# Performance work log

Measured on AMD Instinct MI355X. Metric: run time of the kernel, lower is better.

## Reference

```python
import jax, jax.numpy as jnp
import numpy as np

HEADS = 6
DIM_HEAD = 64
SCALE = DIM_HEAD ** -0.5
BN_EPS = 1e-5


def _dw_pw(x, w_dw, gamma, beta, mean, var, w_pw, stride):
    """Depthwise 3x3 conv (groups=C) -> BatchNorm (inference) -> 1x1 pointwise conv."""
    C = x.shape[1]
    y = jax.lax.conv_general_dilated(
        x, w_dw, window_strides=(stride, stride), padding=((1, 1), (1, 1)),
        dimension_numbers=('NCHW', 'OIHW', 'NCHW'), feature_group_count=C)
    inv = gamma / jnp.sqrt(var + BN_EPS)
    y = y * inv[None, :, None, None] + (beta - mean * inv)[None, :, None, None]
    # 1x1 conv as einsum: w_pw is [O, C]
    return jnp.einsum('bchw,oc->bohw', y, w_pw)


def setup_inputs() -> dict:
    key = jax.random.key(0)
    ks = jax.random.split(key, 10)
    B, C, H, W = 32, 384, 32, 32
    inner = HEADS * DIM_HEAD  # 384
    ws = 0.05  # weight scale to keep attention logits sane
    return {
        'x': jax.random.normal(ks[0], (B, C, H, W), jnp.float32),
        'q_dw': jax.random.normal(ks[1], (C, 1, 3, 3), jnp.float32) * ws,
        'q_gamma': jnp.ones((C,), jnp.float32),
        'q_beta': jnp.zeros((C,), jnp.float32),
        'q_mean': jax.random.normal(ks[2], (C,), jnp.float32) * 0.1,
        'q_var': jax.random.uniform(ks[3], (C,), jnp.float32) + 0.5,
        'q_pw': jax.random.normal(ks[4], (inner, C), jnp.float32) * ws,
        'kv_dw': jax.random.normal(ks[5], (C, 1, 3, 3), jnp.float32) * ws,
        'kv_gamma': jnp.ones((C,), jnp.float32),
        'kv_beta': jnp.zeros((C,), jnp.float32),
        'kv_mean': jax.random.normal(ks[6], (C,), jnp.float32) * 0.1,
        'kv_var': jax.random.uniform(ks[7], (C,), jnp.float32) + 0.5,
        'kv_pw': jax.random.normal(ks[8], (2 * inner, C), jnp.float32) * ws,
        'out_w': jax.random.normal(ks[9], (C, inner), jnp.float32) * ws,
        'out_b': jnp.zeros((C,), jnp.float32),
    }


def reference(x, q_dw, q_gamma, q_beta, q_mean, q_var, q_pw,
              kv_dw, kv_gamma, kv_beta, kv_mean, kv_var, kv_pw,
              out_w, out_b):
    B, C, H, W = x.shape
    h, d = HEADS, DIM_HEAD
    # Q at full resolution, K/V spatially downsampled (stride 2)
    q = _dw_pw(x, q_dw, q_gamma, q_beta, q_mean, q_var, q_pw, stride=1)   # [B, h*d, H, W]
    kv = _dw_pw(x, kv_dw, kv_gamma, kv_beta, kv_mean, kv_var, kv_pw, stride=2)  # [B, 2*h*d, Hk, Wk]
    k, v = jnp.split(kv, 2, axis=1)
    Hk, Wk = k.shape[2], k.shape[3]
    # 'b (h d) x y -> b h (x y) d'
    q = q.reshape(B, h, d, H * W).transpose(0, 1, 3, 2)
    k = k.reshape(B, h, d, Hk * Wk).transpose(0, 1, 3, 2)
    v = v.reshape(B, h, d, Hk * Wk).transpose(0, 1, 3, 2)
    dots = jnp.einsum('bhid,bhjd->bhij', q, k) * SCALE  # [B, h, HW, HkWk]
    attn = jax.nn.softmax(dots, axis=-1)
    out = jnp.einsum('bhij,bhjd->bhid', attn, v)        # [B, h, HW, d]
    # 'b h (x y) d -> b (h d) x y'
    out = out.transpose(0, 1, 3, 2).reshape(B, h * d, H, W)
    # final 1x1 conv projection (dropout is identity, p=0)
    return jnp.einsum('bchw,oc->bohw', out, out_w) + out_b[None, :, None, None]
```

## Files before the change

### kernel.cpp

```cpp
#include <hip/hip_runtime.h>
#include <hip/hip_bf16.h>

#define CIN 384
#define PQ 1024
#define PKV 256
#define HEADS 6
#define DH 64
#define INNER 384
#define ATTN_SCALE 0.125f

typedef __hip_bfloat16 bf16;
typedef unsigned short ushort;
typedef __bf16 bf16x8 __attribute__((ext_vector_type(8)));
typedef float floatx4 __attribute__((ext_vector_type(4)));
typedef short shortx4 __attribute__((ext_vector_type(4)));

#if __has_builtin(__builtin_amdgcn_mfma_f32_16x16x16bf16_1k)
#define HAVE_MFMA16 1
#endif

__device__ __forceinline__ float b2f(bf16 v) { return __bfloat162float(v); }
__device__ __forceinline__ bf16 f2b(float v) { return __float2bfloat16(v); }
__device__ __forceinline__ ushort f2bu(float v) { bf16 h = __float2bfloat16(v); return *(ushort*)&h; }
__device__ __forceinline__ float ldf(const void* p, size_t i, int isbf) {
    return isbf ? __bfloat162float(((const bf16*)p)[i]) : ((const float*)p)[i];
}
__device__ __forceinline__ void dma16(const bf16* g, bf16* l) {
    __builtin_amdgcn_global_load_lds(
        (const __attribute__((address_space(1))) unsigned int*)g,
        (__attribute__((address_space(3))) unsigned int*)l, 16, 0, 0);
}

__global__ void detect_kernel(const unsigned int* __restrict__ x, int* __restrict__ flag) {
    if (threadIdx.x == 0 && blockIdx.x == 0) {
        int cnt = 0;
        for (int i = 0; i < 64; i++) {
            unsigned int e = (x[i] >> 7) & 0xFFu;
            if (e >= 100u && e <= 140u) cnt++;
        }
        *flag = (cnt >= 48) ? 1 : 0;
    }
}

__global__ void wconv_kernel(const void* __restrict__ w0, const void* __restrict__ w1,
                             const void* __restrict__ w2, bf16* __restrict__ dst,
                             const int* __restrict__ flagp) {
    int isbf = *flagp;
    const int n0 = INNER * CIN, n1 = 2 * INNER * CIN, n2 = INNER * CIN;
    int i = blockIdx.x * 256 + threadIdx.x;
    int total = n0 + n1 + n2;
    for (; i < total; i += gridDim.x * 256) {
        float v;
        if (i < n0) v = ldf(w0, i, isbf);
        else if (i < n0 + n1) v = ldf(w1, i - n0, isbf);
        else v = ldf(w2, i - n0 - n1, isbf);
        dst[i] = f2b(v);
    }
}

template <int STRIDE, int HO, int WO>
__global__ __launch_bounds__(256) void dw_bn_kernel(
        const void* __restrict__ x, const void* __restrict__ wdw,
        const void* __restrict__ gamma, const void* __restrict__ beta,
        const void* __restrict__ mean, const void* __restrict__ var,
        bf16* __restrict__ yt, const int* __restrict__ flagp) {
    constexpr int IN_ROWS = (8 - 1) * STRIDE + 3;
    constexpr int RL = 37;
    constexpr int PT = 8 * WO;
    constexpr unsigned XSZ = 32u * IN_ROWS * RL * 4;
    constexpr unsigned OSZ = (unsigned)PT * 40 * 2;
    __shared__ __align__(16) char smem[XSZ > OSZ ? XSZ : OSZ];
    float (*xin)[IN_ROWS][RL] = (float (*)[IN_ROWS][RL])smem;
    ushort (*outt)[40] = (ushort (*)[40])smem;

    int isbf = *flagp;
    int rg = blockIdx.x;
    int c0 = blockIdx.y * 32;
    int b  = blockIdx.z;
    int tid = threadIdx.x;
    int ri0 = rg * 8 * STRIDE - 1;

    for (int e = tid; e < 32 * IN_ROWS; e += 256) {
        int i = e % IN_ROWS, cc = e / IN_ROWS;
        xin[cc][i][0] = 0.f;
        xin[cc][i][33] = 0.f;
    }

    const int NCHUNK = 32 * IN_ROWS * 4;
    for (int ch = tid; ch < NCHUNK; ch += 256) {
        int wc = ch & 3;
        int t  = ch >> 2;
        int i  = t % IN_ROWS;
        int cc = t / IN_ROWS;
        int row = ri0 + i;
        float f[8];
        if (row >= 0 && row < 32) {
            size_t goff = ((size_t)(b * CIN + c0 + cc) * 32 + row) * 32 + wc * 8;
            if (isbf) {
                uint4 v = *(const uint4*)((const bf16*)x + goff);
                const ushort* u = (const ushort*)&v;
#pragma unroll
                for (int j = 0; j < 8; j++) f[j] = __uint_as_float((unsigned)u[j] << 16);
            } else {
                float4 v0 = *(const float4*)((const float*)x + goff);
                float4 v1 = *(const float4*)((const float*)x + goff + 4);
                f[0] = v0.x; f[1] = v0.y; f[2] = v0.z; f[3] = v0.w;
                f[4] = v1.x; f[5] = v1.y; f[6] = v1.z; f[7] = v1.w;
            }
        } else {
#pragma unroll
            for (int j = 0; j < 8; j++) f[j] = 0.f;
        }
        float* dst = &xin[cc][i][1 + wc * 8];
#pragma unroll
        for (int j = 0; j < 8; j++) dst[j] = f[j];
    }

    int cc = tid & 31;
    int g  = tid >> 5;
    int c  = c0 + cc;
    float w9[9];
#pragma unroll
    for (int k = 0; k < 9; k++) w9[k] = ldf(wdw, c * 9 + k, isbf);
    float inv  = ldf(gamma, c, isbf) * rsqrtf(ldf(var, c, isbf) + 1e-5f);
    float bias = ldf(beta, c, isbf) - ldf(mean, c, isbf) * inv;
    __syncthreads();

    const float* xr0 = xin[cc][g * STRIDE + 0];
    const float* xr1 = xin[cc][g * STRIDE + 1];
    const float* xr2 = xin[cc][g * STRIDE + 2];
    float o[WO];
    if (STRIDE == 1) {
        float a0 = xr0[0], a1 = xr0[1];
        float b0 = xr1[0], b1 = xr1[1];
        float q0 = xr2[0], q1 = xr2[1];
#pragma unroll
        for (int wo = 0; wo < WO; wo++) {
            float a2 = xr0[wo + 2], b2 = xr1[wo + 2], q2 = xr2[wo + 2];
            float acc = w9[0] * a0 + w9[1] * a1 + w9[2] * a2
                      + w9[3] * b0 + w9[4] * b1 + w9[5] * b2
                      + w9[6] * q0 + w9[7] * q1 + w9[8] * q2;
            o[wo] = acc * inv + bias;
            a0 = a1; a1 = a2; b0 = b1; b1 = b2; q0 = q1; q1 = q2;
        }
    } else {
        float a0 = xr0[0], b0 = xr1[0], q0 = xr2[0];
#pragma unroll
        for (int wo = 0; wo < WO; wo++) {
            float a1 = xr0[2 * wo + 1], a2 = xr0[2 * wo + 2];
            float b1 = xr1[2 * wo + 1], b2 = xr1[2 * wo + 2];
            float q1 = xr2[2 * wo + 1], q2 = xr2[2 * wo + 2];
            float acc = w9[0] * a0 + w9[1] * a1 + w9[2] * a2
                      + w9[3] * b0 + w9[4] * b1 + w9[5] * b2
                      + w9[6] * q0 + w9[7] * q1 + w9[8] * q2;
            o[wo] = acc * inv + bias;
            a0 = a2; b0 = b2; q0 = q2;
        }
    }
    __syncthreads();

#pragma unroll
    for (int wo = 0; wo < WO; wo++) outt[g * WO + wo][cc] = f2bu(o[wo]);
    __syncthreads();

    const size_t pbase = (size_t)b * (HO * WO) + (size_t)rg * 8 * WO;
    for (int chk = tid; chk < PT * 4; chk += 256) {
        int k = chk & 3, p = chk >> 2;
        uint4 v = *(const uint4*)&outt[p][k * 8];
        *(uint4*)(yt + (pbase + p) * CIN + c0 + k * 8) = v;
    }
}

template <int P, int MODE>
__global__ __launch_bounds__(256, 2) void mfma_pw(
        const bf16* __restrict__ wt, const bf16* __restrict__ yt,
        const void* __restrict__ bias, void* __restrict__ out0,
        bf16* __restrict__ out1, int O, const int* __restrict__ flagp) {
    __shared__ __align__(16) bf16 As[2][4096];
    __shared__ __align__(16) bf16 Bs[2][4096];
    int tid = threadIdx.x;
    int wave = tid >> 6, lane = tid & 63;
    int l15 = lane & 15, quad = lane >> 4;
    int wm = wave & 1, wn = wave >> 1;
    int b = blockIdx.z;
    int p0 = blockIdx.x * 128;
    int o0 = blockIdx.y * 128;

    const bf16* asrc = yt + ((size_t)b * P + p0) * CIN;
    const bf16* bsrc = wt + (size_t)o0 * CIN;

    int srow = (lane >> 2);
    int sc   = lane & 3;
    auto stage = [&](int step, int buf) {
#pragma unroll
        for (int it = 0; it < 2; it++) {
            int row = wave * 32 + it * 16 + srow;
            int g = sc ^ (row & 3);
            size_t goff = (size_t)row * CIN + step * 32 + g * 8;
            dma16(asrc + goff, &As[buf][(wave * 2 + it) * 512]);
            dma16(bsrc + goff, &Bs[buf][(wave * 2 + it) * 512]);
        }
    };

    floatx4 acc[4][4];
#pragma unroll
    for (int pt = 0; pt < 4; pt++)
#pragma unroll
        for (int ot = 0; ot < 4; ot++) acc[pt][ot] = (floatx4){0.f, 0.f, 0.f, 0.f};

    stage(0, 0);
    __syncthreads();
    for (int s = 0; s < CIN / 32; s++) {
        int buf = s & 1;
        if (s < CIN / 32 - 1) stage(s + 1, buf ^ 1);
        bf16x8 af[4], bw[4];
        int slot = (quad ^ (l15 & 3)) * 8;
#pragma unroll
        for (int pt = 0; pt < 4; pt++)
            af[pt] = *(const bf16x8*)&As[buf][(wm * 64 + pt * 16 + l15) * 32 + slot];
#pragma unroll
        for (int ot = 0; ot < 4; ot++)
            bw[ot] = *(const bf16x8*)&Bs[buf][(wn * 64 + ot * 16 + l15) * 32 + slot];
#pragma unroll
        for (int pt = 0; pt < 4; pt++)
#pragma unroll
            for (int ot = 0; ot < 4; ot++)
                acc[pt][ot] = __builtin_amdgcn_mfma_f32_16x16x32_bf16(af[pt], bw[ot], acc[pt][ot], 0, 0, 0);
        __syncthreads();
    }

    int pw0 = p0 + wm * 64, ow0 = o0 + wn * 64;
    if (MODE == 2) {
        int isbf = *flagp;
#pragma unroll
        for (int ot = 0; ot < 4; ot++) {
            int o = ow0 + ot * 16 + l15;
            float bv = ldf(bias, o, isbf);
#pragma unroll
            for (int pt = 0; pt < 4; pt++) {
                int p = pw0 + pt * 16 + quad * 4;
                size_t idx = ((size_t)b * O + o) * P + p;
                if (!isbf) {
                    float4 v4 = {acc[pt][ot][0] + bv, acc[pt][ot][1] + bv,
                                 acc[pt][ot][2] + bv, acc[pt][ot][3] + bv};
                    *(float4*)((float*)out0 + idx) = v4;
                } else {
                    ushort4 u4 = {f2bu(acc[pt][ot][0] + bv), f2bu(acc[pt][ot][1] + bv),
                                  f2bu(acc[pt][ot][2] + bv), f2bu(acc[pt][ot][3] + bv)};
                    *(ushort4*)((bf16*)out0 + idx) = u4;
                }
            }
        }
    } else if (MODE == 0) {
#pragma unroll
        for (int ot = 0; ot < 4; ot++) {
            int o = ow0 + ot * 16 + l15;
            int h = o >> 6, d = o & 63;
            bf16* base = (bf16*)out0 + ((size_t)(b * HEADS + h) * P) * 64 + d;
#pragma unroll
            for (int pt = 0; pt < 4; pt++)
#pragma unroll
                for (int r = 0; r < 4; r++)
                    base[(size_t)(pw0 + pt * 16 + quad * 4 + r) * 64] = f2b(acc[pt][ot][r]);
        }
    } else {
#pragma unroll
        for (int ot = 0; ot < 4; ot++) {
            int o = ow0 + ot * 16 + l15;
            if (o < INNER) {
                int h = o >> 6, d = o & 63;
                bf16* base = (bf16*)out0 + ((size_t)(b * HEADS + h) * P) * 64 + d;
#pragma unroll
                for (int pt = 0; pt < 4; pt++)
#pragma unroll
                    for (int r = 0; r < 4; r++)
                        base[(size_t)(pw0 + pt * 16 + quad * 4 + r) * 64] = f2b(acc[pt][ot][r]);
            } else {
                int ch = o - INNER;
                bf16* base = out1 + ((size_t)b * INNER + ch) * PKV;
#pragma unroll
                for (int pt = 0; pt < 4; pt++)
#pragma unroll
                    for (int r = 0; r < 4; r++)
                        base[pw0 + pt * 16 + quad * 4 + r] = f2b(acc[pt][ot][r]);
            }
        }
    }
}

__global__ __launch_bounds__(256, 2) void attn_kernel(
        const bf16* __restrict__ qalt, const bf16* __restrict__ kalt,
        const bf16* __restrict__ valt, bf16* __restrict__ ao) {
    __shared__ __align__(16) bf16 Kl[16384];
    __shared__ __align__(16) bf16 Vl[16384];
    __shared__ __align__(16) ushort Ot[4][16][80];
    int tid = threadIdx.x;
    int wave = tid >> 6, lane = tid & 63;
    int l15 = lane & 15, quad = lane >> 4;
    int blk = blockIdx.x;
    int swz = (blk & 7) * 96 + (blk >> 3);
    int seg = swz & 3;
    int bh  = swz >> 2;
    int b = bh / HEADS, h = bh % HEADS;

    const bf16* qbase = qalt + (size_t)(b * HEADS + h) * PQ * DH;
    const bf16* kbase = kalt + (size_t)(b * HEADS + h) * PKV * DH;
    const bf16* vbase = valt + ((size_t)b * INNER + h * DH) * PKV;

    {
        int j = lane >> 3, cs = lane & 7;
#pragma unroll
        for (int it = 0; it < 8; it++) {
            int jr = (wave * 8 + it) * 8 + j;
            int g = cs ^ (jr & 7);
            dma16(kbase + (size_t)jr * 64 + g * 8, &Kl[(wave * 8 + it) * 512]);
        }
        int d = lane >> 5, cs2 = lane & 31;
#pragma unroll
        for (int it = 0; it < 8; it++) {
            int dr = (wave * 8 + it) * 2 + d;
            int g = cs2 ^ (dr & 15);
            dma16(vbase + (size_t)dr * 256 + g * 8, &Vl[(wave * 8 + it) * 512]);
        }
    }

    int p0 = seg * 256 + wave * 16;
    const bf16* qrow = qbase + (size_t)(p0 + l15) * DH + quad * 8;
    bf16x8 qc0 = *(const bf16x8*)qrow;
    bf16x8 qc1 = *(const bf16x8*)(qrow + 32);
    __syncthreads();

#pragma unroll
    for (int t = 0; t < 4; t++) {
        bf16x8 qn0 = qc0, qn1 = qc1;
        if (t < 3) {
            const bf16* qr = qrow + (size_t)(t + 1) * 64 * DH;
            qn0 = *(const bf16x8*)qr;
            qn1 = *(const bf16x8*)(qr + 32);
        }

        floatx4 s[16];
#pragma unroll
        for (int jt = 0; jt < 16; jt++) s[jt] = (floatx4){0.f, 0.f, 0.f, 0.f};
#pragma unroll
        for (int jt = 0; jt < 16; jt++) {
            int j = jt * 16 + l15;
            bf16x8 k0 = *(const bf16x8*)&Kl[j * 64 + (quad ^ (j & 7)) * 8];
            bf16x8 k1 = *(const bf16x8*)&Kl[j * 64 + ((4 + quad) ^ (j & 7)) * 8];
            s[jt] = __builtin_amdgcn_mfma_f32_16x16x32_bf16(k0, qc0, s[jt], 0, 0, 0);
            s[jt] = __builtin_amdgcn_mfma_f32_16x16x32_bf16(k1, qc1, s[jt], 0, 0, 0);
        }

        float mx = s[0][0];
#pragma unroll
        for (int jt = 0; jt < 16; jt++)
#pragma unroll
            for (int r = 0; r < 4; r++) mx = fmaxf(mx, s[jt][r]);
        mx = fmaxf(mx, __shfl_xor(mx, 16, 64));
        mx = fmaxf(mx, __shfl_xor(mx, 32, 64));
        float sm = 0.f;
#pragma unroll
        for (int jt = 0; jt < 16; jt++)
#pragma unroll
            for (int r = 0; r < 4; r++) {
                float e = __expf((s[jt][r] - mx) * ATTN_SCALE);
                s[jt][r] = e;
                sm += e;
            }
        sm += __shfl_xor(sm, 16, 64);
        sm += __shfl_xor(sm, 32, 64);
        float pinv = 1.f / sm;

        floatx4 oacc[4];
#pragma unroll
        for (int nt = 0; nt < 4; nt++) oacc[nt] = (floatx4){0.f, 0.f, 0.f, 0.f};
#ifdef HAVE_MFMA16
#pragma unroll
        for (int jt = 0; jt < 16; jt++) {
            shortx4 pa;
#pragma unroll
            for (int r = 0; r < 4; r++) pa[r] = (short)f2bu(s[jt][r] * pinv);
#pragma unroll
            for (int nt = 0; nt < 4; nt++) {
                int d = nt * 16 + l15;
                shortx4 bv = *(const shortx4*)&Vl[d * 256 +
                        ((jt * 2 + (quad >> 1)) ^ (d & 15)) * 8 + (quad & 1) * 4];
                oacc[nt] = __builtin_amdgcn_mfma_f32_16x16x16bf16_1k(pa, bv, oacc[nt], 0, 0, 0);
            }
        }
#else
#pragma unroll
        for (int kk = 0; kk < 8; kk++) {
            unsigned Ad0 = ((unsigned)f2bu(s[2 * kk][1] * pinv) << 16) | f2bu(s[2 * kk][0] * pinv);
            unsigned Ad1 = ((unsigned)f2bu(s[2 * kk][3] * pinv) << 16) | f2bu(s[2 * kk][2] * pinv);
            unsigned Bd0 = ((unsigned)f2bu(s[2 * kk + 1][1] * pinv) << 16) | f2bu(s[2 * kk + 1][0] * pinv);
            unsigned Bd1 = ((unsigned)f2bu(s[2 * kk + 1][3] * pinv) << 16) | f2bu(s[2 * kk + 1][2] * pinv);
            int srcA = l15 + ((quad & 1) << 5);
            unsigned dw[4];
#pragma unroll
            for (int i = 0; i < 4; i++) {
                int srcl = srcA + ((i >> 1) << 4);
                unsigned ta = (i & 1) ? __shfl((int)Ad1, srcl, 64) : __shfl((int)Ad0, srcl, 64);
                unsigned tb = (i & 1) ? __shfl((int)Bd1, srcl, 64) : __shfl((int)Bd0, srcl, 64);
                dw[i] = (quad >> 1) ? tb : ta;
            }
            union { unsigned u[4]; bf16x8 v; } pc;
            pc.u[0] = dw[0]; pc.u[1] = dw[1]; pc.u[2] = dw[2]; pc.u[3] = dw[3];
#pragma unroll
            for (int nt = 0; nt < 4; nt++) {
                int d = nt * 16 + l15;
                bf16x8 bv = *(const bf16x8*)&Vl[d * 256 + ((kk * 4 + quad) ^ (d & 15)) * 8];
                oacc[nt] = __builtin_amdgcn_mfma_f32_16x16x32_bf16(pc.v, bv, oacc[nt], 0, 0, 0);
            }
        }
#endif

#pragma unroll
        for (int nt = 0; nt < 4; nt++)
#pragma unroll
            for (int r = 0; r < 4; r++)
                Ot[wave][quad * 4 + r][nt * 16 + l15] = f2bu(oacc[nt][r]);
        int row = lane >> 2, d0 = (lane & 3) * 16;
        uint4 ld0 = *(const uint4*)&Ot[wave][row][d0];
        uint4 ld1 = *(const uint4*)&Ot[wave][row][d0 + 8];
        bf16* dst = ao + ((size_t)b * PQ + p0 + t * 64 + row) * INNER + h * DH + d0;
        *(uint4*)dst = ld0;
        *(uint4*)(dst + 8) = ld1;

        qc0 = qn0; qc1 = qn1;
    }
}

extern "C" void kernel_launch(void* const* d_in, const int* in_sizes, int n_in,
                              void* d_out, int out_size, void* d_ws, size_t ws_size,
                              hipStream_t stream) {
    const void* x        = d_in[0];
    const void* q_dw     = d_in[1];
    const void* q_gamma  = d_in[2];
    const void* q_beta   = d_in[3];
    const void* q_mean   = d_in[4];
    const void* q_var    = d_in[5];
    const void* q_pw     = d_in[6];
    const void* kv_dw    = d_in[7];
    const void* kv_gamma = d_in[8];
    const void* kv_beta  = d_in[9];
    const void* kv_mean  = d_in[10];
    const void* kv_var   = d_in[11];
    const void* kv_pw    = d_in[12];
    const void* out_w    = d_in[13];
    const void* out_b    = d_in[14];

    int* flag = (int*)d_ws;
    bf16* pool = (bf16*)((char*)d_ws + 256);
    bf16* yqt  = pool;
    bf16* ykvt = yqt  + (size_t)32 * 1024 * 384;
    bf16* qalt = ykvt + (size_t)32 * 256 * 384;
    bf16* kalt = qalt + (size_t)32 * 6 * 1024 * 64;
    bf16* valt = kalt + (size_t)32 * 6 * 256 * 64;
    bf16* wbf  = valt + (size_t)32 * 384 * 256;
    bf16* qpw_bf = wbf;
    bf16* kvpw_bf = wbf + (size_t)INNER * CIN;
    bf16* outw_bf = kvpw_bf + (size_t)2 * INNER * CIN;
    bf16* aob  = yqt;

    detect_kernel<<<1, 64, 0, stream>>>((const unsigned int*)x, flag);
    wconv_kernel<<<576, 256, 0, stream>>>(q_pw, kv_pw, out_w, wbf, flag);
    dw_bn_kernel<1, 32, 32><<<dim3(4, 12, 32), 256, 0, stream>>>(x, q_dw, q_gamma, q_beta, q_mean, q_var, yqt, flag);
    dw_bn_kernel<2, 16, 16><<<dim3(2, 12, 32), 256, 0, stream>>>(x, kv_dw, kv_gamma, kv_beta, kv_mean, kv_var, ykvt, flag);
    mfma_pw<1024, 0><<<dim3(8, 3, 32), 256, 0, stream>>>(qpw_bf, yqt, nullptr, qalt, nullptr, INNER, flag);
    mfma_pw<256, 1><<<dim3(2, 6, 32), 256, 0, stream>>>(kvpw_bf, ykvt, nullptr, kalt, valt, 2 * INNER, flag);
    attn_kernel<<<768, 256, 0, stream>>>(qalt, kalt, valt, aob);
    mfma_pw<1024, 2><<<dim3(8, 3, 32), 256, 0, stream>>>(outw_bf, aob, out_b, d_out, nullptr, CIN, flag);
}
```

Baseline: 241.5 us.

## Inline dtype probe, deepen GEMM K-step, and restructure attention with global K loads

Removes the separate detect kernel and has each kernel run the dtype probe inline, which saves one launch. The pointwise GEMM now stages 64-wide K slices with an 8-way swizzle, halving the number of barrier iterations. The attention kernel drops the K shared-memory copy and reads K straight from global memory. It doubles the grid to 1536 blocks with fewer query tiles each and raises occupancy to 3 blocks per CU. It also switches the softmax to exp2 with a folded scale and packs P using v_cvt_pk_bf16 plus permlane32_swap. The inline probe adds redundant reads of 64 words in every block, and reading K from global memory relies on cache hits.

```diff
diff --git a/kernel.cpp b/kernel.cpp
--- a/kernel.cpp
+++ b/kernel.cpp
@@ -13,11 +13,6 @@
 typedef unsigned short ushort;
 typedef __bf16 bf16x8 __attribute__((ext_vector_type(8)));
 typedef float floatx4 __attribute__((ext_vector_type(4)));
-typedef short shortx4 __attribute__((ext_vector_type(4)));
-
-#if __has_builtin(__builtin_amdgcn_mfma_f32_16x16x16bf16_1k)
-#define HAVE_MFMA16 1
-#endif
 
 __device__ __forceinline__ float b2f(bf16 v) { return __bfloat162float(v); }
 __device__ __forceinline__ bf16 f2b(float v) { return __float2bfloat16(v); }
@@ -30,22 +25,37 @@
         (const __attribute__((address_space(1))) unsigned int*)g,
         (__attribute__((address_space(3))) unsigned int*)l, 16, 0, 0);
 }
-
-__global__ void detect_kernel(const unsigned int* __restrict__ x, int* __restrict__ flag) {
-    if (threadIdx.x == 0 && blockIdx.x == 0) {
-        int cnt = 0;
-        for (int i = 0; i < 64; i++) {
-            unsigned int e = (x[i] >> 7) & 0xFFu;
-            if (e >= 100u && e <= 140u) cnt++;
-        }
-        *flag = (cnt >= 48) ? 1 : 0;
-    }
+__device__ __forceinline__ int probe_isbf(const void* x) {
+    const unsigned* u = (const unsigned*)x;
+    int cnt = 0;
+    for (int i = 0; i < 64; i++) {
+        unsigned e = (u[i] >> 7) & 0xFFu;
+        cnt += (e >= 100u && e <= 140u) ? 1 : 0;
+    }
+    return cnt >= 48 ? 1 : 0;
+}
+__device__ __forceinline__ unsigned cvtpk(float lo, float hi) {
+    unsigned r;
+    asm("v_cvt_pk_bf16_f32 %0, %1, %2" : "=v"(r) : "v"(lo), "v"(hi));
+    return r;
+}
+__device__ __forceinline__ void halfswap(unsigned a, unsigned b, unsigned& lo, unsigned& hi) {
+#if __has_builtin(__builtin_amdgcn_permlane32_swap)
+    auto r = __builtin_amdgcn_permlane32_swap(a, b, false, false);
+    lo = r[0]; hi = r[1];
+#else
+    unsigned ax = (unsigned)__shfl_xor((int)a, 32, 64);
+    unsigned bx = (unsigned)__shfl_xor((int)b, 32, 64);
+    bool lower = (threadIdx.x & 32) == 0;
+    lo = lower ? a : bx;
+    hi = lower ? ax : b;
+#endif
 }
 
 __global__ void wconv_kernel(const void* __restrict__ w0, const void* __restrict__ w1,
                              const void* __restrict__ w2, bf16* __restrict__ dst,
-                             const int* __restrict__ flagp) {
-    int isbf = *flagp;
+                             const void* __restrict__ xprobe) {
+    int isbf = probe_isbf(xprobe);
     const int n0 = INNER * CIN, n1 = 2 * INNER * CIN, n2 = INNER * CIN;
     int i = blockIdx.x * 256 + threadIdx.x;
     int total = n0 + n1 + n2;
@@ -63,7 +73,7 @@
         const void* __restrict__ x, const void* __restrict__ wdw,
         const void* __restrict__ gamma, const void* __restrict__ beta,
         const void* __restrict__ mean, const void* __restrict__ var,
-        bf16* __restrict__ yt, const int* __restrict__ flagp) {
+        bf16* __restrict__ yt) {
     constexpr int IN_ROWS = (8 - 1) * STRIDE + 3;
     constexpr int RL = 37;
     constexpr int PT = 8 * WO;
@@ -73,7 +83,7 @@
     float (*xin)[IN_ROWS][RL] = (float (*)[IN_ROWS][RL])smem;
     ushort (*outt)[40] = (ushort (*)[40])smem;
 
-    int isbf = *flagp;
+    int isbf = probe_isbf(x);
     int rg = blockIdx.x;
     int c0 = blockIdx.y * 32;
     int b  = blockIdx.z;
@@ -175,9 +185,9 @@
 __global__ __launch_bounds__(256, 2) void mfma_pw(
         const bf16* __restrict__ wt, const bf16* __restrict__ yt,
         const void* __restrict__ bias, void* __restrict__ out0,
-        bf16* __restrict__ out1, int O, const int* __restrict__ flagp) {
-    __shared__ __align__(16) bf16 As[2][4096];
-    __shared__ __align__(16) bf16 Bs[2][4096];
+        bf16* __restrict__ out1, int O, const void* __restrict__ xprobe) {
+    __shared__ __align__(16) bf16 As[2][8192];
+    __shared__ __align__(16) bf16 Bs[2][8192];
     int tid = threadIdx.x;
     int wave = tid >> 6, lane = tid & 63;
     int l15 = lane & 15, quad = lane >> 4;
@@ -189,16 +199,16 @@
     const bf16* asrc = yt + ((size_t)b * P + p0) * CIN;
     const bf16* bsrc = wt + (size_t)o0 * CIN;
 
-    int srow = (lane >> 2);
-    int sc   = lane & 3;
+    int srow = lane >> 3;
+    int sc   = lane & 7;
     auto stage = [&](int step, int buf) {
 #pragma unroll
-        for (int it = 0; it < 2; it++) {
-            int row = wave * 32 + it * 16 + srow;
-            int g = sc ^ (row & 3);
-            size_t goff = (size_t)row * CIN + step * 32 + g * 8;
-            dma16(asrc + goff, &As[buf][(wave * 2 + it) * 512]);
-            dma16(bsrc + goff, &Bs[buf][(wave * 2 + it) * 512]);
+        for (int it = 0; it < 4; it++) {
+            int row = wave * 32 + it * 8 + srow;
+            int g = sc ^ (row & 7);
+            size_t goff = (size_t)row * CIN + step * 64 + g * 8;
+            dma16(asrc + goff, &As[buf][(wave * 4 + it) * 512]);
+            dma16(bsrc + goff, &Bs[buf][(wave * 4 + it) * 512]);
         }
     };
 
@@ -210,28 +220,34 @@
 
     stage(0, 0);
     __syncthreads();
-    for (int s = 0; s < CIN / 32; s++) {
+    for (int s = 0; s < CIN / 64; s++) {
         int buf = s & 1;
-        if (s < CIN / 32 - 1) stage(s + 1, buf ^ 1);
-        bf16x8 af[4], bw[4];
-        int slot = (quad ^ (l15 & 3)) * 8;
-#pragma unroll
-        for (int pt = 0; pt < 4; pt++)
-            af[pt] = *(const bf16x8*)&As[buf][(wm * 64 + pt * 16 + l15) * 32 + slot];
-#pragma unroll
-        for (int ot = 0; ot < 4; ot++)
-            bw[ot] = *(const bf16x8*)&Bs[buf][(wn * 64 + ot * 16 + l15) * 32 + slot];
-#pragma unroll
-        for (int pt = 0; pt < 4; pt++)
-#pragma unroll
-            for (int ot = 0; ot < 4; ot++)
-                acc[pt][ot] = __builtin_amdgcn_mfma_f32_16x16x32_bf16(af[pt], bw[ot], acc[pt][ot], 0, 0, 0);
+        if (s < CIN / 64 - 1) stage(s + 1, buf ^ 1);
+#pragma unroll
+        for (int ks = 0; ks < 2; ks++) {
+            bf16x8 af[4], bw[4];
+#pragma unroll
+            for (int pt = 0; pt < 4; pt++) {
+                int row = wm * 64 + pt * 16 + l15;
+                af[pt] = *(const bf16x8*)&As[buf][row * 64 + (((ks * 4 + quad) ^ (row & 7))) * 8];
+            }
+#pragma unroll
+            for (int ot = 0; ot < 4; ot++) {
+                int row = wn * 64 + ot * 16 + l15;
+                bw[ot] = *(const bf16x8*)&Bs[buf][row * 64 + (((ks * 4 + quad) ^ (row & 7))) * 8];
+            }
+#pragma unroll
+            for (int pt = 0; pt < 4; pt++)
+#pragma unroll
+                for (int ot = 0; ot < 4; ot++)
+                    acc[pt][ot] = __builtin_amdgcn_mfma_f32_16x16x32_bf16(af[pt], bw[ot], acc[pt][ot], 0, 0, 0);
+        }
         __syncthreads();
     }
 
     int pw0 = p0 + wm * 64, ow0 = o0 + wn * 64;
     if (MODE == 2) {
-        int isbf = *flagp;
+        int isbf = probe_isbf(xprobe);
 #pragma unroll
         for (int ot = 0; ot < 4; ot++) {
             int o = ow0 + ot * 16 + l15;
@@ -288,19 +304,18 @@
     }
 }
 
-__global__ __launch_bounds__(256, 2) void attn_kernel(
+__global__ __launch_bounds__(256, 3) void attn_kernel(
         const bf16* __restrict__ qalt, const bf16* __restrict__ kalt,
         const bf16* __restrict__ valt, bf16* __restrict__ ao) {
-    __shared__ __align__(16) bf16 Kl[16384];
     __shared__ __align__(16) bf16 Vl[16384];
     __shared__ __align__(16) ushort Ot[4][16][80];
     int tid = threadIdx.x;
     int wave = tid >> 6, lane = tid & 63;
     int l15 = lane & 15, quad = lane >> 4;
     int blk = blockIdx.x;
-    int swz = (blk & 7) * 96 + (blk >> 3);
-    int seg = swz & 3;
-    int bh  = swz >> 2;
+    int swz = (blk & 7) * 192 + (blk >> 3);
+    int seg = swz & 7;
+    int bh  = swz >> 3;
     int b = bh / HEADS, h = bh % HEADS;
 
     const bf16* qbase = qalt + (size_t)(b * HEADS + h) * PQ * DH;
@@ -308,13 +323,6 @@
     const bf16* vbase = valt + ((size_t)b * INNER + h * DH) * PKV;
 
     {
-        int j = lane >> 3, cs = lane & 7;
-#pragma unroll
-        for (int it = 0; it < 8; it++) {
-            int jr = (wave * 8 + it) * 8 + j;
-            int g = cs ^ (jr & 7);
-            dma16(kbase + (size_t)jr * 64 + g * 8, &Kl[(wave * 8 + it) * 512]);
-        }
         int d = lane >> 5, cs2 = lane & 31;
 #pragma unroll
         for (int it = 0; it < 8; it++) {
@@ -324,31 +332,31 @@
         }
     }
 
-    int p0 = seg * 256 + wave * 16;
+    int p0 = seg * 128 + wave * 16;
     const bf16* qrow = qbase + (size_t)(p0 + l15) * DH + quad * 8;
+    const bf16* krow = kbase + (size_t)l15 * DH + quad * 8;
     bf16x8 qc0 = *(const bf16x8*)qrow;
     bf16x8 qc1 = *(const bf16x8*)(qrow + 32);
-    __syncthreads();
-
-#pragma unroll
-    for (int t = 0; t < 4; t++) {
-        bf16x8 qn0 = qc0, qn1 = qc1;
-        if (t < 3) {
-            const bf16* qr = qrow + (size_t)(t + 1) * 64 * DH;
-            qn0 = *(const bf16x8*)qr;
-            qn1 = *(const bf16x8*)(qr + 32);
-        }
-
+
+    const float C = ATTN_SCALE * 1.44269504f;
+
+#pragma unroll
+    for (int t = 0; t < 2; t++) {
         floatx4 s[16];
 #pragma unroll
         for (int jt = 0; jt < 16; jt++) s[jt] = (floatx4){0.f, 0.f, 0.f, 0.f};
 #pragma unroll
         for (int jt = 0; jt < 16; jt++) {
-            int j = jt * 16 + l15;
-            bf16x8 k0 = *(const bf16x8*)&Kl[j * 64 + (quad ^ (j & 7)) * 8];
-            bf16x8 k1 = *(const bf16x8*)&Kl[j * 64 + ((4 + quad) ^ (j & 7)) * 8];
+            bf16x8 k0 = *(const bf16x8*)(krow + jt * 16 * DH);
+            bf16x8 k1 = *(const bf16x8*)(krow + jt * 16 * DH + 32);
             s[jt] = __builtin_amdgcn_mfma_f32_16x16x32_bf16(k0, qc0, s[jt], 0, 0, 0);
             s[jt] = __builtin_amdgcn_mfma_f32_16x16x32_bf16(k1, qc1, s[jt], 0, 0, 0);
+        }
+
+        bf16x8 qn0 = qc0, qn1 = qc1;
+        if (t == 0) {
+            qn0 = *(const bf16x8*)(qrow + 64 * DH);
+            qn1 = *(const bf16x8*)(qrow + 64 * DH + 32);
         }
 
         float mx = s[0][0];
@@ -358,12 +366,13 @@
             for (int r = 0; r < 4; r++) mx = fmaxf(mx, s[jt][r]);
         mx = fmaxf(mx, __shfl_xor(mx, 16, 64));
         mx = fmaxf(mx, __shfl_xor(mx, 32, 64));
+        float mc = mx * C;
         float sm = 0.f;
 #pragma unroll
         for (int jt = 0; jt < 16; jt++)
 #pragma unroll
             for (int r = 0; r < 4; r++) {
-                float e = __expf((s[jt][r] - mx) * ATTN_SCALE);
+                float e = exp2f(s[jt][r] * C - mc);
                 s[jt][r] = e;
                 sm += e;
             }
@@ -371,49 +380,37 @@
         sm += __shfl_xor(sm, 32, 64);
         float pinv = 1.f / sm;
 
+        if (t == 0) __syncthreads();
+
         floatx4 oacc[4];
 #pragma unroll
         for (int nt = 0; nt < 4; nt++) oacc[nt] = (floatx4){0.f, 0.f, 0.f, 0.f};
-#ifdef HAVE_MFMA16
-#pragma unroll
-        for (int jt = 0; jt < 16; jt++) {
-            shortx4 pa;
-#pragma unroll
-            for (int r = 0; r < 4; r++) pa[r] = (short)f2bu(s[jt][r] * pinv);
-#pragma unroll
-            for (int nt = 0; nt < 4; nt++) {
-                int d = nt * 16 + l15;
-                shortx4 bv = *(const shortx4*)&Vl[d * 256 +
-                        ((jt * 2 + (quad >> 1)) ^ (d & 15)) * 8 + (quad & 1) * 4];
-                oacc[nt] = __builtin_amdgcn_mfma_f32_16x16x16bf16_1k(pa, bv, oacc[nt], 0, 0, 0);
-            }
-        }
-#else
 #pragma unroll
         for (int kk = 0; kk < 8; kk++) {
-            unsigned Ad0 = ((unsigned)f2bu(s[2 * kk][1] * pinv) << 16) | f2bu(s[2 * kk][0] * pinv);
-            unsigned Ad1 = ((unsigned)f2bu(s[2 * kk][3] * pinv) << 16) | f2bu(s[2 * kk][2] * pinv);
-            unsigned Bd0 = ((unsigned)f2bu(s[2 * kk + 1][1] * pinv) << 16) | f2bu(s[2 * kk + 1][0] * pinv);
-            unsigned Bd1 = ((unsigned)f2bu(s[2 * kk + 1][3] * pinv) << 16) | f2bu(s[2 * kk + 1][2] * pinv);
-            int srcA = l15 + ((quad & 1) << 5);
-            unsigned dw[4];
-#pragma unroll
-            for (int i = 0; i < 4; i++) {
-                int srcl = srcA + ((i >> 1) << 4);
-                unsigned ta = (i & 1) ? __shfl((int)Ad1, srcl, 64) : __shfl((int)Ad0, srcl, 64);
-                unsigned tb = (i & 1) ? __shfl((int)Bd1, srcl, 64) : __shfl((int)Bd0, srcl, 64);
-                dw[i] = (quad >> 1) ? tb : ta;
-            }
-            union { unsigned u[4]; bf16x8 v; } pc;
-            pc.u[0] = dw[0]; pc.u[1] = dw[1]; pc.u[2] = dw[2]; pc.u[3] = dw[3];
+            floatx4 se = s[2 * kk], so = s[2 * kk + 1];
+            unsigned E0 = cvtpk(se[0] * pinv, se[1] * pinv);
+            unsigned E1 = cvtpk(se[2] * pinv, se[3] * pinv);
+            unsigned D0 = cvtpk(so[0] * pinv, so[1] * pinv);
+            unsigned D1 = cvtpk(so[2] * pinv, so[3] * pinv);
+            unsigned lo0, hi0, lo1, hi1;
+            halfswap(E0, D0, lo0, hi0);
+            halfswap(E1, D1, lo1, hi1);
+            unsigned sel0 = (quad & 1) ? hi0 : lo0;
+            unsigned sel1 = (quad & 1) ? hi1 : lo1;
+            unsigned x0 = (unsigned)__shfl_xor((int)sel0, 16, 64);
+            unsigned x1 = (unsigned)__shfl_xor((int)sel1, 16, 64);
+            union { unsigned u[4]; bf16x8 v; } pf;
+            pf.u[0] = (quad & 1) ? x0 : sel0;
+            pf.u[1] = (quad & 1) ? x1 : sel1;
+            pf.u[2] = (quad & 1) ? sel0 : x0;
+            pf.u[3] = (quad & 1) ? sel1 : x1;
 #pragma unroll
             for (int nt = 0; nt < 4; nt++) {
                 int d = nt * 16 + l15;
                 bf16x8 bv = *(const bf16x8*)&Vl[d * 256 + ((kk * 4 + quad) ^ (d & 15)) * 8];
-                oacc[nt] = __builtin_amdgcn_mfma_f32_16x16x32_bf16(pc.v, bv, oacc[nt], 0, 0, 0);
-            }
-        }
-#endif
+                oacc[nt] = __builtin_amdgcn_mfma_f32_16x16x32_bf16(pf.v, bv, oacc[nt], 0, 0, 0);
+            }
+        }
 
 #pragma unroll
         for (int nt = 0; nt < 4; nt++)
@@ -450,7 +447,6 @@
     const void* out_w    = d_in[13];
     const void* out_b    = d_in[14];
 
-    int* flag = (int*)d_ws;
     bf16* pool = (bf16*)((char*)d_ws + 256);
     bf16* yqt  = pool;
     bf16* ykvt = yqt  + (size_t)32 * 1024 * 384;
@@ -463,12 +459,11 @@
     bf16* outw_bf = kvpw_bf + (size_t)2 * INNER * CIN;
     bf16* aob  = yqt;
 
-    detect_kernel<<<1, 64, 0, stream>>>((const unsigned int*)x, flag);
-    wconv_kernel<<<576, 256, 0, stream>>>(q_pw, kv_pw, out_w, wbf, flag);
-    dw_bn_kernel<1, 32, 32><<<dim3(4, 12, 32), 256, 0, stream>>>(x, q_dw, q_gamma, q_beta, q_mean, q_var, yqt, flag);
-    dw_bn_kernel<2, 16, 16><<<dim3(2, 12, 32), 256, 0, stream>>>(x, kv_dw, kv_gamma, kv_beta, kv_mean, kv_var, ykvt, flag);
-    mfma_pw<1024, 0><<<dim3(8, 3, 32), 256, 0, stream>>>(qpw_bf, yqt, nullptr, qalt, nullptr, INNER, flag);
-    mfma_pw<256, 1><<<dim3(2, 6, 32), 256, 0, stream>>>(kvpw_bf, ykvt, nullptr, kalt, valt, 2 * INNER, flag);
-    attn_kernel<<<768, 256, 0, stream>>>(qalt, kalt, valt, aob);
-    mfma_pw<1024, 2><<<dim3(8, 3, 32), 256, 0, stream>>>(outw_bf, aob, out_b, d_out, nullptr, CIN, flag);
-}
+    wconv_kernel<<<576, 256, 0, stream>>>(q_pw, kv_pw, out_w, wbf, x);
+    dw_bn_kernel<1, 32, 32><<<dim3(4, 12, 32), 256, 0, stream>>>(x, q_dw, q_gamma, q_beta, q_mean, q_var, yqt);
+    dw_bn_kernel<2, 16, 16><<<dim3(2, 12, 32), 256, 0, stream>>>(x, kv_dw, kv_gamma, kv_beta, kv_mean, kv_var, ykvt);
+    mfma_pw<1024, 0><<<dim3(8, 3, 32), 256, 0, stream>>>(qpw_bf, yqt, nullptr, qalt, nullptr, INNER, x);
+    mfma_pw<256, 1><<<dim3(2, 6, 32), 256, 0, stream>>>(kvpw_bf, ykvt, nullptr, kalt, valt, 2 * INNER, x);
+    attn_kernel<<<1536, 256, 0, stream>>>(qalt, kalt, valt, aob);
+    mfma_pw<1024, 2><<<dim3(8, 3, 32), 256, 0, stream>>>(outw_bf, aob, out_b, d_out, nullptr, CIN, x);
+}
```

Result: slower. 263.5 us (+9.1%).
